# Kernel optimization log

Measured on AMD Instinct MI355X. Metric: run time of the kernel, lower is better.

Reference implementation:

```python
import jax, jax.numpy as jnp
import numpy as np


def setup_inputs() -> dict:
    key = jax.random.key(0)
    ks = jax.random.split(key, 12)
    C, H, L, P = 256, 8, 4, 4
    Lq, Lx = 2048, 300
    iss = jnp.array([[64, 64], [32, 32], [16, 16], [8, 8]], dtype=jnp.int32)
    Len_in = int(np.sum(np.array(iss)[:, 0] * np.array(iss)[:, 1]))  # 5440
    lsi = jnp.array([0, 4096, 5120, 5376], dtype=jnp.int32)
    return {
        "query": jax.random.normal(ks[0], (1, Lq, C), jnp.float32),
        "reference_points": jax.random.uniform(ks[1], (1, Lq, L, 2), jnp.float32),
        "input_flatten": jax.random.normal(ks[2], (1, Len_in, C), jnp.float32),
        "input_spatial_shapes": iss,
        "add_keys": jax.random.normal(ks[3], (1, Lx, C), jnp.float32),
        "input_level_start_index": lsi,
        "W_off": jax.random.normal(ks[4], (H * L * P * 2, C), jnp.float32) * 0.01,
        "b_off": jax.random.normal(ks[5], (H * L * P * 2,), jnp.float32),
        "W_attn": jax.random.normal(ks[6], (H * (L + 1), C, C), jnp.float32) * 0.05,
        "W_v": jax.random.normal(ks[7], (H * 2, C, C), jnp.float32) * 0.05,
        "b_v": jax.random.normal(ks[8], (H * 2, C), jnp.float32) * 0.01,
        "W_mix": jax.random.normal(ks[9], (C, H + 1), jnp.float32) * 0.5,
    }


def reference(query, reference_points, input_flatten, input_spatial_shapes,
              add_keys, input_level_start_index, W_off, b_off, W_attn, W_v, b_v, W_mix):
    N, Lq, C = query.shape
    L = input_spatial_shapes.shape[0]
    H = W_v.shape[0] // 2
    P = W_off.shape[0] // (H * L * 2)

    # sampling locations: ref (x,y in [0,1]) + offsets / (W,H)
    off = (query @ W_off.T + b_off).reshape(N, Lq, H, L, P, 2)
    wh = input_spatial_shapes[:, ::-1].astype(query.dtype)  # (L,2) = (W,H)
    loc = reference_points[:, :, None, :, None, :] + off / wh[None, None, None, :, None, :]

    # get_keys: truncating index computation + gather (faithful to original)
    loc = jnp.clip(loc, 0.0, 0.999)
    iss_f = input_spatial_shapes.astype(loc.dtype)[None, None, None, :, None, :]
    idx = (loc * iss_f).astype(jnp.int32)  # (N,Lq,H,L,P,2): (int(x*H_l), int(y*W_l))
    lin = (idx[..., 0]
           + idx[..., 1] * input_spatial_shapes[:, 0].astype(jnp.int32)[None, None, None, :, None]
           + input_level_start_index.astype(jnp.int32)[None, None, None, :, None])
    keys = input_flatten[0][lin[0]]                # (Lq,H,L,P,C)
    keys = jnp.transpose(keys, (1, 2, 3, 0, 4))    # (H,L,P,Lq,C)

    head_w = jax.nn.softmax(W_mix.T, axis=0)       # (H+1,C)
    qf = query[0]                                  # (Lq,C)
    ak = add_keys[0]                               # (Lx,C)

    # per-head, per-level similarity (replicates original overlapping index h*L+lvl)
    Ws = W_attn[jnp.arange(H)[:, None] * L + jnp.arange(L)[None, :]]  # (H,L,C,C)
    T = jnp.einsum('hlce,hlpqe->hlcpq', Ws, keys)  # (H,L,C,P,Lq)
    # faithful reshape quirk: (C, P*Lq) viewed as (P, Lq, C)
    T = T.reshape(H, L, P, Lq, C)
    attn_s = jnp.einsum('hlpqc,qc->hlpq', T, qf).reshape(H, L * P, Lq)

    Wadd = W_attn[jnp.arange(H) * L + L]           # (H,C,C)
    attn_a = jnp.einsum('xe,hce,qc->hxq', ak, Wadd, qf)  # (H,Lx,Lq)

    attn = jax.nn.softmax(jnp.concatenate([attn_s, attn_a], axis=1), axis=1)
    attn_s_sm, attn_a_sm = attn[:, :L * P], attn[:, L * P:]

    Wv0, bv0 = W_v[0::2], b_v[0::2]
    Wv1, bv1 = W_v[1::2], b_v[1::2]
    vals = (jnp.einsum('hlpqe,hce->hlpqc', keys, Wv0)
            + bv0[:, None, None, None, :]).reshape(H, L * P, Lq, C)
    v2 = jnp.einsum('xe,hce->hxc', ak, Wv1) + bv1[:, None, :]  # (H,Lx,C)

    out_h = (jnp.einsum('hkq,hkqc->hqc', attn_s_sm, vals)
             + jnp.einsum('hxq,hxc->hqc', attn_a_sm, v2))      # (H,Lq,C)
    result = qf * head_w[-1][None, :] + jnp.einsum('hqc,hc->qc', out_h, head_w[:-1])
    return result[None]
```

## Files before the change

### kernel.cpp

```cpp
#include <hip/hip_runtime.h>
#include <stdint.h>

#define NJ 316

typedef __attribute__((ext_vector_type(8))) short short8;
typedef __attribute__((ext_vector_type(4))) float f32x4;
union U4S8 { uint4 u; short8 s; };

__device__ __forceinline__ unsigned short f2bf(float x) {
    unsigned int u = __float_as_uint(x);
    u += 0x7fff + ((u >> 16) & 1);
    return (unsigned short)(u >> 16);
}
__device__ __forceinline__ float bf2f(unsigned short h) {
    return __uint_as_float(((unsigned int)h) << 16);
}

__global__ __launch_bounds__(256) void cvt_all_kernel(
    const float* __restrict__ q,  unsigned short* __restrict__ qh,  unsigned short* __restrict__ ql,
    const float* __restrict__ ak, unsigned short* __restrict__ akh, unsigned short* __restrict__ akl,
    const float* __restrict__ wv, unsigned short* __restrict__ wvh, unsigned short* __restrict__ wvl,
    const float* __restrict__ inflat, unsigned int* __restrict__ inflatP,
    const float* __restrict__ Wattn, unsigned short* __restrict__ wah, unsigned short* __restrict__ wal,
    unsigned short* __restrict__ v2th, unsigned short* __restrict__ v2tl)
{
    int i = blockIdx.x * 256 + threadIdx.x;
    if (i < 760576) {
        const float* s; unsigned short *dh, *dl; int off; bool pack = false;
        unsigned int* dp = nullptr;
        if (i < 131072)      { s = q;  dh = qh;  dl = ql;  off = i; }
        else if (i < 150272) { s = ak; dh = akh; dl = akl; off = i - 131072; }
        else if (i < 412416) { s = wv; dh = wvh; dl = wvl; off = i - 150272; }
        else { s = inflat; dp = inflatP; off = i - 412416; pack = true; dh = dl = nullptr; }
        float4 v = ((const float4*)s)[off];
        float x[4] = {v.x, v.y, v.z, v.w};
        unsigned short h[4], l[4];
        #pragma unroll
        for (int j = 0; j < 4; ++j) {
            h[j] = f2bf(x[j]);
            l[j] = f2bf(x[j] - bf2f(h[j]));
        }
        if (pack) {
            ((uint4*)dp)[off] = make_uint4(
                (unsigned)h[0] | ((unsigned)l[0] << 16),
                (unsigned)h[1] | ((unsigned)l[1] << 16),
                (unsigned)h[2] | ((unsigned)l[2] << 16),
                (unsigned)h[3] | ((unsigned)l[3] << 16));
        } else {
            ((uint2*)dh)[off] = make_uint2((unsigned)h[0] | ((unsigned)h[1] << 16),
                                           (unsigned)h[2] | ((unsigned)h[3] << 16));
            ((uint2*)dl)[off] = make_uint2((unsigned)l[0] | ((unsigned)l[1] << 16),
                                           (unsigned)l[2] | ((unsigned)l[3] << 16));
        }
    } else if (i < 891648) {
        int off = i - 760576;
        int base = off * 4;
        int z = base >> 16, r = base & 65535;
        float4 v = *(const float4*)&Wattn[(size_t)(4 * z + 4) * 65536 + r];
        float x[4] = {v.x, v.y, v.z, v.w};
        unsigned short h[4], l[4];
        #pragma unroll
        for (int j = 0; j < 4; ++j) {
            h[j] = f2bf(x[j]);
            l[j] = f2bf(x[j] - bf2f(h[j]));
        }
        ((uint2*)wah)[off] = make_uint2((unsigned)h[0] | ((unsigned)h[1] << 16),
                                        (unsigned)h[2] | ((unsigned)h[3] << 16));
        ((uint2*)wal)[off] = make_uint2((unsigned)l[0] | ((unsigned)l[1] << 16),
                                        (unsigned)l[2] | ((unsigned)l[3] << 16));
    } else {
        int j = i - 891648;
        size_t base = (size_t)j * 320;
        uint2 zz = make_uint2(0u, 0u);
        #pragma unroll
        for (int d = 0; d < 4; ++d) {
            ((uint2*)(v2th + base))[d] = zz;
            ((uint2*)(v2tl + base))[d] = zz;
        }
        ((uint2*)(v2th + base + 316))[0] = zz;
        ((uint2*)(v2tl + base + 316))[0] = zz;
    }
}

__global__ __launch_bounds__(256) void lin_kernel(
    const float* __restrict__ query, const float* __restrict__ refp,
    const int* __restrict__ iss, const int* __restrict__ lsi,
    const float* __restrict__ Woff, const float* __restrict__ boff,
    int* __restrict__ lin)
{
    __shared__ float qf8[8][256];
    __shared__ float wtile[256][33];
    __shared__ double offl[8][256];
    const int t = threadIdx.x;
    const int qbase = blockIdx.x * 8;
    #pragma unroll
    for (int i = 0; i < 8; ++i) qf8[i][t] = query[(qbase + i) * 256 + t];
    double acc[8];
    #pragma unroll
    for (int r = 0; r < 8; ++r) acc[r] = 0.0;
    for (int cb = 0; cb < 256; cb += 32) {
        __syncthreads();
        #pragma unroll
        for (int i = 0; i < 32; ++i) {
            int f = i * 256 + t;
            int o = f >> 5, jj = f & 31;
            wtile[o][jj] = Woff[o * 256 + cb + jj];
        }
        __syncthreads();
        #pragma unroll
        for (int jj = 0; jj < 32; ++jj) {
            double wv = (double)wtile[t][jj];
            #pragma unroll
            for (int r = 0; r < 8; ++r)
                acc[r] += (double)qf8[r][cb + jj] * wv;
        }
    }
    double bo = (double)boff[t];
    __syncthreads();
    #pragma unroll
    for (int r = 0; r < 8; ++r) offl[r][t] = acc[r] + bo;
    __syncthreads();
    #pragma unroll
    for (int rep = 0; rep < 4; ++rep) {
        int idx = rep * 256 + t;
        int r = idx >> 7;
        int s = idx & 127;
        int l = (s >> 2) & 3;
        int q = qbase + r;
        double offx = offl[r][2 * s];
        double offy = offl[r][2 * s + 1];
        int w0 = iss[l * 2 + 0];
        int w1 = iss[l * 2 + 1];
        double locx = (double)refp[q * 8 + l * 2 + 0] + offx / (double)w1;
        double locy = (double)refp[q * 8 + l * 2 + 1] + offy / (double)w0;
        locx = fmin(fmax(locx, 0.0), 0.999);
        locy = fmin(fmax(locy, 0.0), 0.999);
        int ix = (int)(locx * (double)w0);
        int iy = (int)(locy * (double)w1);
        lin[q * 128 + s] = ix + iy * w0 + lsi[l];
    }
}

__global__ __launch_bounds__(256, 2) void gattn_mfma(
    const unsigned short* __restrict__ qh, const unsigned short* __restrict__ ql,
    const unsigned int* __restrict__ inflatP, const float* __restrict__ Wattn,
    const int* __restrict__ lin, float* __restrict__ attn)
{
    __shared__ int linrow[256];
    __shared__ float Glds[64][268];
    const int t = threadIdx.x;
    const int lane = t & 63, w = t >> 6;
    const int b = blockIdx.x;
    const int qb = b & 7, p = (b >> 3) & 3, l = (b >> 5) & 3, h = b >> 7;
    linrow[t] = lin[(256 * qb + t) * 128 + h * 16 + l * 4 + p];
    __syncthreads();

    const int l15 = lane & 15, g = lane >> 4;
    const int q2l = qb + 8 * p + 32 * l15;
    const int ebase = 64 * w + l15;

    f32x4 acc[4][4];
    #pragma unroll
    for (int i = 0; i < 4; ++i)
        #pragma unroll
        for (int eg = 0; eg < 4; ++eg) acc[i][eg] = (f32x4){0.f, 0.f, 0.f, 0.f};

    for (int kb = 0; kb < 256; kb += 32) {
        U4S8 ah[4], al[4];
        #pragma unroll
        for (int i = 0; i < 4; ++i) {
            size_t off = (size_t)(q2l + 512 * i) * 256 + kb + 8 * g;
            ah[i].u = *(const uint4*)(qh + off);
            al[i].u = *(const uint4*)(ql + off);
        }
        int rowoff[8];
        #pragma unroll
        for (int m = 0; m < 8; ++m) rowoff[m] = linrow[kb + 8 * g + m] * 256;
        unsigned int uv[4][8];
        #pragma unroll
        for (int eg = 0; eg < 4; ++eg)
            #pragma unroll
            for (int m = 0; m < 8; ++m)
                uv[eg][m] = inflatP[rowoff[m] + ebase + 16 * eg];

        #pragma unroll
        for (int eg = 0; eg < 4; ++eg) {
            U4S8 bh, bl;
            unsigned int hh[4], ll[4];
            #pragma unroll
            for (int d = 0; d < 4; ++d) {
                hh[d] = __builtin_amdgcn_perm(uv[eg][2 * d + 1], uv[eg][2 * d],
                                              0x05040100u);
                ll[d] = __builtin_amdgcn_perm(uv[eg][2 * d + 1], uv[eg][2 * d],
                                              0x07060302u);
            }
            bh.u = make_uint4(hh[0], hh[1], hh[2], hh[3]);
            bl.u = make_uint4(ll[0], ll[1], ll[2], ll[3]);
            #pragma unroll
            for (int i = 0; i < 4; ++i) {
                acc[i][eg] = __builtin_amdgcn_mfma_f32_16x16x32_bf16(
                    ah[i].s, bh.s, acc[i][eg], 0, 0, 0);
                acc[i][eg] = __builtin_amdgcn_mfma_f32_16x16x32_bf16(
                    ah[i].s, bl.s, acc[i][eg], 0, 0, 0);
                acc[i][eg] = __builtin_amdgcn_mfma_f32_16x16x32_bf16(
                    al[i].s, bh.s, acc[i][eg], 0, 0, 0);
            }
        }
    }

    #pragma unroll
    for (int i = 0; i < 4; ++i)
        #pragma unroll
        for (int eg = 0; eg < 4; ++eg)
            #pragma unroll
            for (int r = 0; r < 4; ++r)
                Glds[16 * i + 4 * g + r][64 * w + 16 * eg + l15] = acc[i][eg][r];
    __syncthreads();

    const int tx = t & 15, ty = t >> 4;
    const float* Wsbase = Wattn + (size_t)(h * 4 + l) * 65536;
    float gv[4][16];
    #pragma unroll
    for (int r = 0; r < 4; ++r)
        #pragma unroll
        for (int i2 = 0; i2 < 4; ++i2) {
            float4 gd = *(const float4*)&Glds[ty * 4 + r][tx * 4 + 64 * i2];
            gv[r][i2 * 4 + 0] = gd.x;
            gv[r][i2 * 4 + 1] = gd.y;
            gv[r][i2 * 4 + 2] = gd.z;
            gv[r][i2 * 4 + 3] = gd.w;
        }
    #pragma unroll
    for (int r = 0; r < 4; ++r) {
        int hi = ty * 4 + r;
        int q2 = qb + 8 * p + 32 * hi;
        #pragma unroll
        for (int p2 = 0; p2 < 4; ++p2) {
            const float* wr = Wsbase + (size_t)(hi + 64 * p2) * 256;
            float partial = 0.f;
            #pragma unroll
            for (int i2 = 0; i2 < 4; ++i2) {
                float4 wv = *(const float4*)&wr[tx * 4 + 64 * i2];
                partial += wv.x * gv[r][i2 * 4 + 0] + wv.y * gv[r][i2 * 4 + 1]
                         + wv.z * gv[r][i2 * 4 + 2] + wv.w * gv[r][i2 * 4 + 3];
            }
            partial += __shfl_xor(partial, 1);
            partial += __shfl_xor(partial, 2);
            partial += __shfl_xor(partial, 4);
            partial += __shfl_xor(partial, 8);
            if (tx == 0)
                attn[((size_t)h * 2048 + q2) * NJ + (l * 4 + p2)] = partial;
        }
    }
}

struct Seg {
    const unsigned short *Ah, *Al, *Bh, *Bl;
    int K, lda, ldb;
    long sA, sB;
    int nprod;
};

template<bool ACCUM, bool OUTF32, int NSEG>
__device__ __forceinline__ void gemm_core(
    const Seg& s0, const Seg& s1,
    float* __restrict__ Cf, unsigned short* __restrict__ Ch,
    unsigned short* __restrict__ Cl,
    int M, int N, int ldc, long sC, int nb, int mb, int z)
{
    __shared__ unsigned short As[2][64 * 40];
    __shared__ unsigned short Bs[2][128 * 40];
    const int t = threadIdx.x;
    const int lane = t & 63;
    const int wave = t >> 6;
    const int wm = (wave & 1) * 32, wn = (wave >> 1) * 64;

    f32x4 acc[2][4];
    #pragma unroll
    for (int i = 0; i < 2; ++i)
        #pragma unroll
        for (int j = 0; j < 4; ++j) acc[i][j] = (f32x4){0.f, 0.f, 0.f, 0.f};

    const int arow = t >> 2, akoff = (t & 3) * 8;
    const int frow = lane & 15, fk = (lane >> 4) * 8;

    #pragma unroll
    for (int seg = 0; seg < NSEG; ++seg) {
        const Seg S = seg ? s1 : s0;
        const int np = S.nprod;
        const unsigned short* Azh = S.Ah + (size_t)z * S.sA;
        const unsigned short* Azl = (np >= 2) ? S.Al + (size_t)z * S.sA : nullptr;
        const unsigned short* Bzh = S.Bh + (size_t)z * S.sB;
        const unsigned short* Bzl = (np >= 3) ? S.Bl + (size_t)z * S.sB : nullptr;
        for (int kb = 0; kb < S.K; kb += 32) {
            __syncthreads();
            {
                int gm = mb + arow;
                uint4 vh = {0, 0, 0, 0}, vl = {0, 0, 0, 0};
                if (gm < M) {
                    size_t o = (size_t)gm * S.lda + kb + akoff;
                    vh = *(const uint4*)(Azh + o);
                    if (np >= 2) vl = *(const uint4*)(Azl + o);
                }
                *(uint4*)&As[0][arow * 40 + akoff] = vh;
                if (np >= 2) *(uint4*)&As[1][arow * 40 + akoff] = vl;
                #pragma unroll
                for (int i = 0; i < 2; ++i) {
                    int f = i * 256 + t;
                    int brow = f >> 2, bkoff = (f & 3) * 8;
                    int gn = nb + brow;
                    uint4 wh = {0, 0, 0, 0}, wl = {0, 0, 0, 0};
                    if (gn < N) {
                        size_t o = (size_t)gn * S.ldb + kb + bkoff;
                        wh = *(const uint4*)(Bzh + o);
                        if (np >= 3) wl = *(const uint4*)(Bzl + o);
                    }
                    *(uint4*)&Bs[0][brow * 40 + bkoff] = wh;
                    if (np >= 3) *(uint4*)&Bs[1][brow * 40 + bkoff] = wl;
                }
            }
            __syncthreads();
            short8 a[2][2], b[4][2];
            #pragma unroll
            for (int i = 0; i < 2; ++i) {
                int r = wm + i * 16 + frow;
                a[i][0] = *(const short8*)&As[0][r * 40 + fk];
                if (np >= 2) a[i][1] = *(const short8*)&As[1][r * 40 + fk];
            }
            #pragma unroll
            for (int j = 0; j < 4; ++j) {
                int r = wn + j * 16 + frow;
                b[j][0] = *(const short8*)&Bs[0][r * 40 + fk];
                if (np >= 3) b[j][1] = *(const short8*)&Bs[1][r * 40 + fk];
            }
            #pragma unroll
            for (int i = 0; i < 2; ++i)
                #pragma unroll
                for (int j = 0; j < 4; ++j) {
                    acc[i][j] = __builtin_amdgcn_mfma_f32_16x16x32_bf16(
                        a[i][0], b[j][0], acc[i][j], 0, 0, 0);
                    if (np >= 2)
                        acc[i][j] = __builtin_amdgcn_mfma_f32_16x16x32_bf16(
                            a[i][1], b[j][0], acc[i][j], 0, 0, 0);
                    if (np >= 3)
                        acc[i][j] = __builtin_amdgcn_mfma_f32_16x16x32_bf16(
                            a[i][0], b[j][1], acc[i][j], 0, 0, 0);
                }
        }
    }
    #pragma unroll
    for (int i = 0; i < 2; ++i)
        #pragma unroll
        for (int r = 0; r < 4; ++r) {
            int gm = mb + wm + i * 16 + (lane >> 4) * 4 + r;
            if (gm >= M) continue;
            #pragma unroll
            for (int j = 0; j < 4; ++j) {
                int gn = nb + wn + j * 16 + (lane & 15);
                if (gn >= N) continue;
                size_t idx = (size_t)z * sC + (size_t)gm * ldc + gn;
                float v = acc[i][j][r];
                if (OUTF32) {
                    float prev = ACCUM ? Cf[idx] : 0.f;
                    Cf[idx] = prev + v;
                } else {
                    unsigned short h = f2bf(v);
                    Ch[idx] = h;
                    Cl[idx] = f2bf(v - bf2f(h));
                }
            }
        }
}

template<bool ACCUM, bool OUTF32, int NSEG>
__global__ __launch_bounds__(256) void mfma_gemm(
    Seg s0, Seg s1,
    float* __restrict__ Cf, unsigned short* __restrict__ Ch,
    unsigned short* __restrict__ Cl,
    int M, int N, int ldc, long sC)
{
    gemm_core<ACCUM, OUTF32, NSEG>(s0, s1, Cf, Ch, Cl, M, N, ldc, sC,
                                   blockIdx.x * 128, blockIdx.y * 64,
                                   blockIdx.z);
}

__global__ __launch_bounds__(256) void mfma_gemm_dual(
    Seg a, int Ma, int Na, int ldca, long sCa,
    unsigned short* __restrict__ Cha, unsigned short* __restrict__ Cla,
    Seg b, int Mb, int Nb, int ldcb, long sCb,
    unsigned short* __restrict__ Chb, unsigned short* __restrict__ Clb,
    int ax)
{
    Seg dummy = a;
    if ((int)blockIdx.x < ax) {
        if ((int)blockIdx.y * 64 >= Ma) return;
        gemm_core<false, false, 1>(a, dummy, nullptr, Cha, Cla,
                                   Ma, Na, ldca, sCa,
                                   blockIdx.x * 128, blockIdx.y * 64,
                                   blockIdx.z);
    } else {
        if ((int)blockIdx.y * 64 >= Mb) return;
        gemm_core<false, false, 1>(b, dummy, nullptr, Chb, Clb,
                                   Mb, Nb, ldcb, sCb,
                                   (blockIdx.x - ax) * 128, blockIdx.y * 64,
                                   blockIdx.z);
    }
}

__global__ __launch_bounds__(256) void softmax_ka_kernel(
    const float* __restrict__ attn, const unsigned int* __restrict__ inflatP,
    const int* __restrict__ lin, float* __restrict__ s0,
    unsigned short* __restrict__ awh,
    unsigned short* __restrict__ KAh, unsigned short* __restrict__ KAl)
{
    __shared__ float red[8];
    __shared__ float w16[16];
    __shared__ int lls[16];
    const int t = threadIdx.x;
    const int lane = t & 63, w = t >> 6;
    const int rid = blockIdx.x;
    const int h = rid >> 11, q = rid & 2047;
    const float* row = attn + (size_t)rid * NJ;

    float v0 = row[t];
    float v1 = (t < 60) ? row[256 + t] : -1e30f;
    float m = fmaxf(v0, v1);
    #pragma unroll
    for (int d = 1; d < 64; d <<= 1) m = fmaxf(m, __shfl_xor(m, d));
    if (lane == 0) red[w] = m;
    __syncthreads();
    m = fmaxf(fmaxf(red[0], red[1]), fmaxf(red[2], red[3]));

    float e0 = expf(v0 - m);
    float e1 = (t < 60) ? expf(v1 - m) : 0.f;
    float s = e0 + e1;
    #pragma unroll
    for (int d = 1; d < 64; d <<= 1) s += __shfl_xor(s, d);
    if (lane == 0) red[4 + w] = s;
    __syncthreads();
    s = (red[4] + red[5]) + (red[6] + red[7]);
    const float inv = 1.f / s;

    float sf = (t < 16) ? e0 : 0.f;
    #pragma unroll
    for (int d = 1; d < 64; d <<= 1) sf += __shfl_xor(sf, d);
    if (lane == 0) red[w] = sf;

    float a0 = e0 * inv;
    float a1 = (t < 60) ? e1 * inv : 0.f;
    awh[(size_t)rid * 320 + t] = f2bf(a0);
    if (t < 64)
        awh[(size_t)rid * 320 + 256 + t] = f2bf(a1);
    if (t < 16) {
        w16[t] = a0;
        lls[t] = lin[q * 128 + h * 16 + t];
    }
    __syncthreads();
    if (t == 0)
        s0[rid] = ((red[0] + red[1]) + (red[2] + red[3])) * inv;

    float acc = 0.f;
    #pragma unroll
    for (int k = 0; k < 16; ++k) {
        unsigned int u = inflatP[lls[k] * 256 + t];
        acc += w16[k] * (bf2f((unsigned short)(u & 0xffff)) +
                         bf2f((unsigned short)(u >> 16)));
    }
    unsigned short hh = f2bf(acc);
    KAh[(size_t)rid * 256 + t] = hh;
    KAl[(size_t)rid * 256 + t] = f2bf(acc - bf2f(hh));
}

__global__ __launch_bounds__(256) void final_kernel(
    const float* __restrict__ qf, const float* __restrict__ OH,
    const float* __restrict__ s0, const float* __restrict__ bv,
    const float* __restrict__ Wmix, float* __restrict__ out)
{
    const int q = blockIdx.x, c = threadIdx.x;
    float wj[9], m = -1e30f;
    #pragma unroll
    for (int j = 0; j < 9; ++j) { wj[j] = Wmix[c * 9 + j]; m = fmaxf(m, wj[j]); }
    float s = 0.f;
    #pragma unroll
    for (int j = 0; j < 9; ++j) { wj[j] = expf(wj[j] - m); s += wj[j]; }
    float inv = 1.f / s;
    float acc = qf[q * 256 + c] * wj[8] * inv;
    #pragma unroll
    for (int h = 0; h < 8; ++h) {
        float s0v = s0[h * 2048 + q];
        float oh = OH[((size_t)h * 2048 + q) * 256 + c]
                 + s0v * bv[(2 * h) * 256 + c]
                 + (1.f - s0v) * bv[(2 * h + 1) * 256 + c];
        acc += oh * wj[h] * inv;
    }
    out[q * 256 + c] = acc;
}

extern "C" void kernel_launch(void* const* d_in, const int* in_sizes, int n_in,
                              void* d_out, int out_size, void* d_ws, size_t ws_size,
                              hipStream_t stream) {
    const float* query = (const float*)d_in[0];
    const float* refp  = (const float*)d_in[1];
    const float* inflat= (const float*)d_in[2];
    const int*   iss   = (const int*)d_in[3];
    const float* ak    = (const float*)d_in[4];
    const int*   lsi   = (const int*)d_in[5];
    const float* Woff  = (const float*)d_in[6];
    const float* boff  = (const float*)d_in[7];
    const float* Wattn = (const float*)d_in[8];
    const float* Wv    = (const float*)d_in[9];
    const float* bv    = (const float*)d_in[10];
    const float* Wmix  = (const float*)d_in[11];
    float* out = (float*)d_out;

    typedef unsigned short us;
    char* ws = (char*)d_ws;
    int* lin    = (int*)ws;   ws += (size_t)262144 * 4;
    float* attn = (float*)ws; ws += (size_t)8 * 2048 * NJ * 4;
    float* s0   = (float*)ws; ws += (size_t)8 * 2048 * 4;
    unsigned int* inflatP = (unsigned int*)ws; ws += (size_t)1392640 * 4;
    us* qh  = (us*)ws; ws += (size_t)524288 * 2;
    us* ql  = (us*)ws; ws += (size_t)524288 * 2;
    us* akh = (us*)ws; ws += (size_t)320 * 256 * 2;
    us* akl = (us*)ws; ws += (size_t)320 * 256 * 2;
    us* Waddh = (us*)ws; ws += (size_t)524288 * 2;
    us* Waddl = (us*)ws; ws += (size_t)524288 * 2;
    us* Wvh = (us*)ws; ws += (size_t)1048576 * 2;
    us* Wvl = (us*)ws; ws += (size_t)1048576 * 2;
    us* Bhh = (us*)ws; ws += (size_t)8 * 320 * 256 * 2;
    us* Bhl = (us*)ws; ws += (size_t)8 * 320 * 256 * 2;
    us* V2Th= (us*)ws; ws += (size_t)8 * 256 * 320 * 2;
    us* V2Tl= (us*)ws; ws += (size_t)8 * 256 * 320 * 2;
    us* awh = (us*)ws; ws += (size_t)8 * 2048 * 320 * 2;
    us* KAh = (us*)ws; ws += (size_t)8 * 2048 * 256 * 2;
    us* KAl = (us*)ws; ws += (size_t)8 * 2048 * 256 * 2;
    float* OH = (float*)ws;   ws += (size_t)8 * 2048 * 256 * 4;

    cvt_all_kernel<<<3491, 256, 0, stream>>>(
        query, qh, ql, ak, akh, akl, Wv, Wvh, Wvl,
        inflat, inflatP, Wattn, Waddh, Waddl, V2Th, V2Tl);
    lin_kernel<<<256, 256, 0, stream>>>(query, refp, iss, lsi, Woff, boff, lin);

    Seg sz = {nullptr, nullptr, nullptr, nullptr, 0, 0, 0, 0L, 0L, 0};

    {
        Seg a = {akh, akl, Waddh, Waddl, 256, 256, 256, 0L, 65536L, 3};
        Seg b = {Wvh + 65536, Wvl + 65536, akh, nullptr, 256, 256, 256,
                 131072L, 0L, 2};
        mfma_gemm_dual<<<dim3(5, 5, 8), 256, 0, stream>>>(
            a, 300, 256, 256, 320L * 256, Bhh, Bhl,
            b, 256, 300, 320, 256L * 320, V2Th + 16, V2Tl + 16, 2);
    }
    {
        Seg a = {qh, ql, Bhh, Bhl, 256, 256, 256, 0L, 320L * 256, 3};
        mfma_gemm<false, true, 1><<<dim3(3, 32, 8), 256, 0, stream>>>(
            a, sz, attn + 16, nullptr, nullptr, 2048, 300, NJ, 2048L * NJ);
    }

    gattn_mfma<<<1024, 256, 0, stream>>>(qh, ql, inflatP, Wattn, lin, attn);

    softmax_ka_kernel<<<16384, 256, 0, stream>>>(attn, inflatP, lin, s0,
                                                 awh, KAh, KAl);

    {
        Seg a = {KAh, KAl, Wvh, nullptr, 256, 256, 256, 2048L * 256,
                 2L * 65536, 2};
        Seg b = {awh, nullptr, V2Th, nullptr, 320, 320, 320, 2048L * 320,
                 256L * 320, 1};
        mfma_gemm<false, true, 2><<<dim3(2, 32, 8), 256, 0, stream>>>(
            a, b, OH, nullptr, nullptr, 2048, 256, 256, 2048L * 256);
    }

    final_kernel<<<2048, 256, 0, stream>>>(query, OH, s0, bv, Wmix, out);
}
```

Before: 268.7 us.

## Merge conversion with offset kernel and gather-attn with attn-add GEMM launches

The conversion kernel and the sampling-offset kernel become one launch, with extra blocks running the offset/lin computation. The gather-attention kernel and the attn-add GEMM are also combined into a single launch of 1792 blocks, using shared memory passed into gemm_core. This removes two launches and lets independent work overlap within one grid. The cost is that the shared-memory allocation (69.6KB) applies to every block, including GEMM blocks, which may cut occupancy. The offset kernel's weight tile was also halved to 16 columns.

```diff
diff --git a/kernel.cpp b/kernel.cpp
--- a/kernel.cpp
+++ b/kernel.cpp
@@ -14,244 +14,6 @@
 }
 __device__ __forceinline__ float bf2f(unsigned short h) {
     return __uint_as_float(((unsigned int)h) << 16);
-}
-
-__global__ __launch_bounds__(256) void cvt_all_kernel(
-    const float* __restrict__ q,  unsigned short* __restrict__ qh,  unsigned short* __restrict__ ql,
-    const float* __restrict__ ak, unsigned short* __restrict__ akh, unsigned short* __restrict__ akl,
-    const float* __restrict__ wv, unsigned short* __restrict__ wvh, unsigned short* __restrict__ wvl,
-    const float* __restrict__ inflat, unsigned int* __restrict__ inflatP,
-    const float* __restrict__ Wattn, unsigned short* __restrict__ wah, unsigned short* __restrict__ wal,
-    unsigned short* __restrict__ v2th, unsigned short* __restrict__ v2tl)
-{
-    int i = blockIdx.x * 256 + threadIdx.x;
-    if (i < 760576) {
-        const float* s; unsigned short *dh, *dl; int off; bool pack = false;
-        unsigned int* dp = nullptr;
-        if (i < 131072)      { s = q;  dh = qh;  dl = ql;  off = i; }
-        else if (i < 150272) { s = ak; dh = akh; dl = akl; off = i - 131072; }
-        else if (i < 412416) { s = wv; dh = wvh; dl = wvl; off = i - 150272; }
-        else { s = inflat; dp = inflatP; off = i - 412416; pack = true; dh = dl = nullptr; }
-        float4 v = ((const float4*)s)[off];
-        float x[4] = {v.x, v.y, v.z, v.w};
-        unsigned short h[4], l[4];
-        #pragma unroll
-        for (int j = 0; j < 4; ++j) {
-            h[j] = f2bf(x[j]);
-            l[j] = f2bf(x[j] - bf2f(h[j]));
-        }
-        if (pack) {
-            ((uint4*)dp)[off] = make_uint4(
-                (unsigned)h[0] | ((unsigned)l[0] << 16),
-                (unsigned)h[1] | ((unsigned)l[1] << 16),
-                (unsigned)h[2] | ((unsigned)l[2] << 16),
-                (unsigned)h[3] | ((unsigned)l[3] << 16));
-        } else {
-            ((uint2*)dh)[off] = make_uint2((unsigned)h[0] | ((unsigned)h[1] << 16),
-                                           (unsigned)h[2] | ((unsigned)h[3] << 16));
-            ((uint2*)dl)[off] = make_uint2((unsigned)l[0] | ((unsigned)l[1] << 16),
-                                           (unsigned)l[2] | ((unsigned)l[3] << 16));
-        }
-    } else if (i < 891648) {
-        int off = i - 760576;
-        int base = off * 4;
-        int z = base >> 16, r = base & 65535;
-        float4 v = *(const float4*)&Wattn[(size_t)(4 * z + 4) * 65536 + r];
-        float x[4] = {v.x, v.y, v.z, v.w};
-        unsigned short h[4], l[4];
-        #pragma unroll
-        for (int j = 0; j < 4; ++j) {
-            h[j] = f2bf(x[j]);
-            l[j] = f2bf(x[j] - bf2f(h[j]));
-        }
-        ((uint2*)wah)[off] = make_uint2((unsigned)h[0] | ((unsigned)h[1] << 16),
-                                        (unsigned)h[2] | ((unsigned)h[3] << 16));
-        ((uint2*)wal)[off] = make_uint2((unsigned)l[0] | ((unsigned)l[1] << 16),
-                                        (unsigned)l[2] | ((unsigned)l[3] << 16));
-    } else {
-        int j = i - 891648;
-        size_t base = (size_t)j * 320;
-        uint2 zz = make_uint2(0u, 0u);
-        #pragma unroll
-        for (int d = 0; d < 4; ++d) {
-            ((uint2*)(v2th + base))[d] = zz;
-            ((uint2*)(v2tl + base))[d] = zz;
-        }
-        ((uint2*)(v2th + base + 316))[0] = zz;
-        ((uint2*)(v2tl + base + 316))[0] = zz;
-    }
-}
-
-__global__ __launch_bounds__(256) void lin_kernel(
-    const float* __restrict__ query, const float* __restrict__ refp,
-    const int* __restrict__ iss, const int* __restrict__ lsi,
-    const float* __restrict__ Woff, const float* __restrict__ boff,
-    int* __restrict__ lin)
-{
-    __shared__ float qf8[8][256];
-    __shared__ float wtile[256][33];
-    __shared__ double offl[8][256];
-    const int t = threadIdx.x;
-    const int qbase = blockIdx.x * 8;
-    #pragma unroll
-    for (int i = 0; i < 8; ++i) qf8[i][t] = query[(qbase + i) * 256 + t];
-    double acc[8];
-    #pragma unroll
-    for (int r = 0; r < 8; ++r) acc[r] = 0.0;
-    for (int cb = 0; cb < 256; cb += 32) {
-        __syncthreads();
-        #pragma unroll
-        for (int i = 0; i < 32; ++i) {
-            int f = i * 256 + t;
-            int o = f >> 5, jj = f & 31;
-            wtile[o][jj] = Woff[o * 256 + cb + jj];
-        }
-        __syncthreads();
-        #pragma unroll
-        for (int jj = 0; jj < 32; ++jj) {
-            double wv = (double)wtile[t][jj];
-            #pragma unroll
-            for (int r = 0; r < 8; ++r)
-                acc[r] += (double)qf8[r][cb + jj] * wv;
-        }
-    }
-    double bo = (double)boff[t];
-    __syncthreads();
-    #pragma unroll
-    for (int r = 0; r < 8; ++r) offl[r][t] = acc[r] + bo;
-    __syncthreads();
-    #pragma unroll
-    for (int rep = 0; rep < 4; ++rep) {
-        int idx = rep * 256 + t;
-        int r = idx >> 7;
-        int s = idx & 127;
-        int l = (s >> 2) & 3;
-        int q = qbase + r;
-        double offx = offl[r][2 * s];
-        double offy = offl[r][2 * s + 1];
-        int w0 = iss[l * 2 + 0];
-        int w1 = iss[l * 2 + 1];
-        double locx = (double)refp[q * 8 + l * 2 + 0] + offx / (double)w1;
-        double locy = (double)refp[q * 8 + l * 2 + 1] + offy / (double)w0;
-        locx = fmin(fmax(locx, 0.0), 0.999);
-        locy = fmin(fmax(locy, 0.0), 0.999);
-        int ix = (int)(locx * (double)w0);
-        int iy = (int)(locy * (double)w1);
-        lin[q * 128 + s] = ix + iy * w0 + lsi[l];
-    }
-}
-
-__global__ __launch_bounds__(256, 2) void gattn_mfma(
-    const unsigned short* __restrict__ qh, const unsigned short* __restrict__ ql,
-    const unsigned int* __restrict__ inflatP, const float* __restrict__ Wattn,
-    const int* __restrict__ lin, float* __restrict__ attn)
-{
-    __shared__ int linrow[256];
-    __shared__ float Glds[64][268];
-    const int t = threadIdx.x;
-    const int lane = t & 63, w = t >> 6;
-    const int b = blockIdx.x;
-    const int qb = b & 7, p = (b >> 3) & 3, l = (b >> 5) & 3, h = b >> 7;
-    linrow[t] = lin[(256 * qb + t) * 128 + h * 16 + l * 4 + p];
-    __syncthreads();
-
-    const int l15 = lane & 15, g = lane >> 4;
-    const int q2l = qb + 8 * p + 32 * l15;
-    const int ebase = 64 * w + l15;
-
-    f32x4 acc[4][4];
-    #pragma unroll
-    for (int i = 0; i < 4; ++i)
-        #pragma unroll
-        for (int eg = 0; eg < 4; ++eg) acc[i][eg] = (f32x4){0.f, 0.f, 0.f, 0.f};
-
-    for (int kb = 0; kb < 256; kb += 32) {
-        U4S8 ah[4], al[4];
-        #pragma unroll
-        for (int i = 0; i < 4; ++i) {
-            size_t off = (size_t)(q2l + 512 * i) * 256 + kb + 8 * g;
-            ah[i].u = *(const uint4*)(qh + off);
-            al[i].u = *(const uint4*)(ql + off);
-        }
-        int rowoff[8];
-        #pragma unroll
-        for (int m = 0; m < 8; ++m) rowoff[m] = linrow[kb + 8 * g + m] * 256;
-        unsigned int uv[4][8];
-        #pragma unroll
-        for (int eg = 0; eg < 4; ++eg)
-            #pragma unroll
-            for (int m = 0; m < 8; ++m)
-                uv[eg][m] = inflatP[rowoff[m] + ebase + 16 * eg];
-
-        #pragma unroll
-        for (int eg = 0; eg < 4; ++eg) {
-            U4S8 bh, bl;
-            unsigned int hh[4], ll[4];
-            #pragma unroll
-            for (int d = 0; d < 4; ++d) {
-                hh[d] = __builtin_amdgcn_perm(uv[eg][2 * d + 1], uv[eg][2 * d],
-                                              0x05040100u);
-                ll[d] = __builtin_amdgcn_perm(uv[eg][2 * d + 1], uv[eg][2 * d],
-                                              0x07060302u);
-            }
-            bh.u = make_uint4(hh[0], hh[1], hh[2], hh[3]);
-            bl.u = make_uint4(ll[0], ll[1], ll[2], ll[3]);
-            #pragma unroll
-            for (int i = 0; i < 4; ++i) {
-                acc[i][eg] = __builtin_amdgcn_mfma_f32_16x16x32_bf16(
-                    ah[i].s, bh.s, acc[i][eg], 0, 0, 0);
-                acc[i][eg] = __builtin_amdgcn_mfma_f32_16x16x32_bf16(
-                    ah[i].s, bl.s, acc[i][eg], 0, 0, 0);
-                acc[i][eg] = __builtin_amdgcn_mfma_f32_16x16x32_bf16(
-                    al[i].s, bh.s, acc[i][eg], 0, 0, 0);
-            }
-        }
-    }
-
-    #pragma unroll
-    for (int i = 0; i < 4; ++i)
-        #pragma unroll
-        for (int eg = 0; eg < 4; ++eg)
-            #pragma unroll
-            for (int r = 0; r < 4; ++r)
-                Glds[16 * i + 4 * g + r][64 * w + 16 * eg + l15] = acc[i][eg][r];
-    __syncthreads();
-
-    const int tx = t & 15, ty = t >> 4;
-    const float* Wsbase = Wattn + (size_t)(h * 4 + l) * 65536;
-    float gv[4][16];
-    #pragma unroll
-    for (int r = 0; r < 4; ++r)
-        #pragma unroll
-        for (int i2 = 0; i2 < 4; ++i2) {
-            float4 gd = *(const float4*)&Glds[ty * 4 + r][tx * 4 + 64 * i2];
-            gv[r][i2 * 4 + 0] = gd.x;
-            gv[r][i2 * 4 + 1] = gd.y;
-            gv[r][i2 * 4 + 2] = gd.z;
-            gv[r][i2 * 4 + 3] = gd.w;
-        }
-    #pragma unroll
-    for (int r = 0; r < 4; ++r) {
-        int hi = ty * 4 + r;
-        int q2 = qb + 8 * p + 32 * hi;
-        #pragma unroll
-        for (int p2 = 0; p2 < 4; ++p2) {
-            const float* wr = Wsbase + (size_t)(hi + 64 * p2) * 256;
-            float partial = 0.f;
-            #pragma unroll
-            for (int i2 = 0; i2 < 4; ++i2) {
-                float4 wv = *(const float4*)&wr[tx * 4 + 64 * i2];
-                partial += wv.x * gv[r][i2 * 4 + 0] + wv.y * gv[r][i2 * 4 + 1]
-                         + wv.z * gv[r][i2 * 4 + 2] + wv.w * gv[r][i2 * 4 + 3];
-            }
-            partial += __shfl_xor(partial, 1);
-            partial += __shfl_xor(partial, 2);
-            partial += __shfl_xor(partial, 4);
-            partial += __shfl_xor(partial, 8);
-            if (tx == 0)
-                attn[((size_t)h * 2048 + q2) * NJ + (l * 4 + p2)] = partial;
-        }
-    }
 }
 
 struct Seg {
@@ -266,10 +28,10 @@
     const Seg& s0, const Seg& s1,
     float* __restrict__ Cf, unsigned short* __restrict__ Ch,
     unsigned short* __restrict__ Cl,
-    int M, int N, int ldc, long sC, int nb, int mb, int z)
-{
-    __shared__ unsigned short As[2][64 * 40];
-    __shared__ unsigned short Bs[2][128 * 40];
+    int M, int N, int ldc, long sC, int nb, int mb, int z, char* smem)
+{
+    unsigned short* As0 = (unsigned short*)smem;
+    unsigned short* Bs0 = (unsigned short*)(smem + 10240);
     const int t = threadIdx.x;
     const int lane = t & 63;
     const int wave = t >> 6;
@@ -302,8 +64,8 @@
                     vh = *(const uint4*)(Azh + o);
                     if (np >= 2) vl = *(const uint4*)(Azl + o);
                 }
-                *(uint4*)&As[0][arow * 40 + akoff] = vh;
-                if (np >= 2) *(uint4*)&As[1][arow * 40 + akoff] = vl;
+                *(uint4*)&As0[arow * 40 + akoff] = vh;
+                if (np >= 2) *(uint4*)&As0[2560 + arow * 40 + akoff] = vl;
                 #pragma unroll
                 for (int i = 0; i < 2; ++i) {
                     int f = i * 256 + t;
@@ -315,8 +77,8 @@
                         wh = *(const uint4*)(Bzh + o);
                         if (np >= 3) wl = *(const uint4*)(Bzl + o);
                     }
-                    *(uint4*)&Bs[0][brow * 40 + bkoff] = wh;
-                    if (np >= 3) *(uint4*)&Bs[1][brow * 40 + bkoff] = wl;
+                    *(uint4*)&Bs0[brow * 40 + bkoff] = wh;
+                    if (np >= 3) *(uint4*)&Bs0[5120 + brow * 40 + bkoff] = wl;
                 }
             }
             __syncthreads();
@@ -324,14 +86,14 @@
             #pragma unroll
             for (int i = 0; i < 2; ++i) {
                 int r = wm + i * 16 + frow;
-                a[i][0] = *(const short8*)&As[0][r * 40 + fk];
-                if (np >= 2) a[i][1] = *(const short8*)&As[1][r * 40 + fk];
+                a[i][0] = *(const short8*)&As0[r * 40 + fk];
+                if (np >= 2) a[i][1] = *(const short8*)&As0[2560 + r * 40 + fk];
             }
             #pragma unroll
             for (int j = 0; j < 4; ++j) {
                 int r = wn + j * 16 + frow;
-                b[j][0] = *(const short8*)&Bs[0][r * 40 + fk];
-                if (np >= 3) b[j][1] = *(const short8*)&Bs[1][r * 40 + fk];
+                b[j][0] = *(const short8*)&Bs0[r * 40 + fk];
+                if (np >= 3) b[j][1] = *(const short8*)&Bs0[5120 + r * 40 + fk];
             }
             #pragma unroll
             for (int i = 0; i < 2; ++i)
@@ -379,9 +141,10 @@
     unsigned short* __restrict__ Cl,
     int M, int N, int ldc, long sC)
 {
+    __shared__ __align__(16) char smem[30720];
     gemm_core<ACCUM, OUTF32, NSEG>(s0, s1, Cf, Ch, Cl, M, N, ldc, sC,
                                    blockIdx.x * 128, blockIdx.y * 64,
-                                   blockIdx.z);
+                                   blockIdx.z, smem);
 }
 
 __global__ __launch_bounds__(256) void mfma_gemm_dual(
@@ -391,19 +154,269 @@
     unsigned short* __restrict__ Chb, unsigned short* __restrict__ Clb,
     int ax)
 {
+    __shared__ __align__(16) char smem[30720];
     Seg dummy = a;
     if ((int)blockIdx.x < ax) {
         if ((int)blockIdx.y * 64 >= Ma) return;
         gemm_core<false, false, 1>(a, dummy, nullptr, Cha, Cla,
                                    Ma, Na, ldca, sCa,
                                    blockIdx.x * 128, blockIdx.y * 64,
-                                   blockIdx.z);
+                                   blockIdx.z, smem);
     } else {
         if ((int)blockIdx.y * 64 >= Mb) return;
         gemm_core<false, false, 1>(b, dummy, nullptr, Chb, Clb,
                                    Mb, Nb, ldcb, sCb,
                                    (blockIdx.x - ax) * 128, blockIdx.y * 64,
-                                   blockIdx.z);
+                                   blockIdx.z, smem);
+    }
+}
+
+__global__ __launch_bounds__(256) void cvt_lin_kernel(
+    const float* __restrict__ q,  unsigned short* __restrict__ qh,  unsigned short* __restrict__ ql,
+    const float* __restrict__ ak, unsigned short* __restrict__ akh, unsigned short* __restrict__ akl,
+    const float* __restrict__ wv, unsigned short* __restrict__ wvh, unsigned short* __restrict__ wvl,
+    const float* __restrict__ inflat, unsigned int* __restrict__ inflatP,
+    const float* __restrict__ Wattn, unsigned short* __restrict__ wah, unsigned short* __restrict__ wal,
+    unsigned short* __restrict__ v2th, unsigned short* __restrict__ v2tl,
+    const float* __restrict__ refp, const int* __restrict__ iss,
+    const int* __restrict__ lsi, const float* __restrict__ Woff,
+    const float* __restrict__ boff, int* __restrict__ lin)
+{
+    __shared__ float qf8[8][256];
+    __shared__ float wtile[256][17];
+    __shared__ double offl[8][256];
+    const int t = threadIdx.x;
+
+    if (blockIdx.x < 3491) {
+        int i = blockIdx.x * 256 + t;
+        if (i < 760576) {
+            const float* s; unsigned short *dh, *dl; int off; bool pack = false;
+            unsigned int* dp = nullptr;
+            if (i < 131072)      { s = q;  dh = qh;  dl = ql;  off = i; }
+            else if (i < 150272) { s = ak; dh = akh; dl = akl; off = i - 131072; }
+            else if (i < 412416) { s = wv; dh = wvh; dl = wvl; off = i - 150272; }
+            else { s = inflat; dp = inflatP; off = i - 412416; pack = true; dh = dl = nullptr; }
+            float4 v = ((const float4*)s)[off];
+            float x[4] = {v.x, v.y, v.z, v.w};
+            unsigned short h[4], l[4];
+            #pragma unroll
+            for (int j = 0; j < 4; ++j) {
+                h[j] = f2bf(x[j]);
+                l[j] = f2bf(x[j] - bf2f(h[j]));
+            }
+            if (pack) {
+                ((uint4*)dp)[off] = make_uint4(
+                    (unsigned)h[0] | ((unsigned)l[0] << 16),
+                    (unsigned)h[1] | ((unsigned)l[1] << 16),
+                    (unsigned)h[2] | ((unsigned)l[2] << 16),
+                    (unsigned)h[3] | ((unsigned)l[3] << 16));
+            } else {
+                ((uint2*)dh)[off] = make_uint2((unsigned)h[0] | ((unsigned)h[1] << 16),
+                                               (unsigned)h[2] | ((unsigned)h[3] << 16));
+                ((uint2*)dl)[off] = make_uint2((unsigned)l[0] | ((unsigned)l[1] << 16),
+                                               (unsigned)l[2] | ((unsigned)l[3] << 16));
+            }
+        } else if (i < 891648) {
+            int off = i - 760576;
+            int base = off * 4;
+            int z = base >> 16, r = base & 65535;
+            float4 v = *(const float4*)&Wattn[(size_t)(4 * z + 4) * 65536 + r];
+            float x[4] = {v.x, v.y, v.z, v.w};
+            unsigned short h[4], l[4];
+            #pragma unroll
+            for (int j = 0; j < 4; ++j) {
+                h[j] = f2bf(x[j]);
+                l[j] = f2bf(x[j] - bf2f(h[j]));
+            }
+            ((uint2*)wah)[off] = make_uint2((unsigned)h[0] | ((unsigned)h[1] << 16),
+                                            (unsigned)h[2] | ((unsigned)h[3] << 16));
+            ((uint2*)wal)[off] = make_uint2((unsigned)l[0] | ((unsigned)l[1] << 16),
+                                            (unsigned)l[2] | ((unsigned)l[3] << 16));
+        } else {
+            int j = i - 891648;
+            size_t base = (size_t)j * 320;
+            uint2 zz = make_uint2(0u, 0u);
+            #pragma unroll
+            for (int d = 0; d < 4; ++d) {
+                ((uint2*)(v2th + base))[d] = zz;
+                ((uint2*)(v2tl + base))[d] = zz;
+            }
+            ((uint2*)(v2th + base + 316))[0] = zz;
+            ((uint2*)(v2tl + base + 316))[0] = zz;
+        }
+        return;
+    }
+
+    const int qbase = (blockIdx.x - 3491) * 8;
+    #pragma unroll
+    for (int i = 0; i < 8; ++i) qf8[i][t] = q[(qbase + i) * 256 + t];
+    double acc[8];
+    #pragma unroll
+    for (int r = 0; r < 8; ++r) acc[r] = 0.0;
+    for (int cb = 0; cb < 256; cb += 16) {
+        __syncthreads();
+        #pragma unroll
+        for (int i = 0; i < 16; ++i) {
+            int f = i * 256 + t;
+            int o = f >> 4, jj = f & 15;
+            wtile[o][jj] = Woff[o * 256 + cb + jj];
+        }
+        __syncthreads();
+        #pragma unroll
+        for (int jj = 0; jj < 16; ++jj) {
+            double wvv = (double)wtile[t][jj];
+            #pragma unroll
+            for (int r = 0; r < 8; ++r)
+                acc[r] += (double)qf8[r][cb + jj] * wvv;
+        }
+    }
+    double bo = (double)boff[t];
+    __syncthreads();
+    #pragma unroll
+    for (int r = 0; r < 8; ++r) offl[r][t] = acc[r] + bo;
+    __syncthreads();
+    #pragma unroll
+    for (int rep = 0; rep < 4; ++rep) {
+        int idx = rep * 256 + t;
+        int r = idx >> 7;
+        int s = idx & 127;
+        int l = (s >> 2) & 3;
+        int qq = qbase + r;
+        double offx = offl[r][2 * s];
+        double offy = offl[r][2 * s + 1];
+        int w0 = iss[l * 2 + 0];
+        int w1 = iss[l * 2 + 1];
+        double locx = (double)refp[qq * 8 + l * 2 + 0] + offx / (double)w1;
+        double locy = (double)refp[qq * 8 + l * 2 + 1] + offy / (double)w0;
+        locx = fmin(fmax(locx, 0.0), 0.999);
+        locy = fmin(fmax(locy, 0.0), 0.999);
+        int ix = (int)(locx * (double)w0);
+        int iy = (int)(locy * (double)w1);
+        lin[qq * 128 + s] = ix + iy * w0 + lsi[l];
+    }
+}
+
+__global__ __launch_bounds__(256, 2) void gattn_attnA(
+    const unsigned short* __restrict__ qh, const unsigned short* __restrict__ ql,
+    const unsigned int* __restrict__ inflatP, const float* __restrict__ Wattn,
+    const int* __restrict__ lin, float* __restrict__ attn, Seg aA)
+{
+    __shared__ __align__(16) char smem[69632];
+    const int t = threadIdx.x;
+
+    if ((int)blockIdx.x >= 1024) {
+        int idx = blockIdx.x - 1024;
+        int z = idx & 7, my = (idx >> 3) & 31, nx = idx >> 8;
+        gemm_core<false, true, 1>(aA, aA, attn + 16, nullptr, nullptr,
+                                  2048, 300, NJ, 2048L * NJ,
+                                  nx * 128, my * 64, z, smem);
+        return;
+    }
+
+    int* linrow = (int*)smem;
+    float (*Glds)[268] = (float(*)[268])(smem + 1024);
+    const int lane = t & 63, w = t >> 6;
+    const int b = blockIdx.x;
+    const int qb = b & 7, p = (b >> 3) & 3, l = (b >> 5) & 3, h = b >> 7;
+    linrow[t] = lin[(256 * qb + t) * 128 + h * 16 + l * 4 + p];
+    __syncthreads();
+
+    const int l15 = lane & 15, g = lane >> 4;
+    const int q2l = qb + 8 * p + 32 * l15;
+    const int ebase = 64 * w + l15;
+
+    f32x4 acc[4][4];
+    #pragma unroll
+    for (int i = 0; i < 4; ++i)
+        #pragma unroll
+        for (int eg = 0; eg < 4; ++eg) acc[i][eg] = (f32x4){0.f, 0.f, 0.f, 0.f};
+
+    for (int kb = 0; kb < 256; kb += 32) {
+        U4S8 ah[4], al[4];
+        #pragma unroll
+        for (int i = 0; i < 4; ++i) {
+            size_t off = (size_t)(q2l + 512 * i) * 256 + kb + 8 * g;
+            ah[i].u = *(const uint4*)(qh + off);
+            al[i].u = *(const uint4*)(ql + off);
+        }
+        int rowoff[8];
+        #pragma unroll
+        for (int m = 0; m < 8; ++m) rowoff[m] = linrow[kb + 8 * g + m] * 256;
+        unsigned int uv[4][8];
+        #pragma unroll
+        for (int eg = 0; eg < 4; ++eg)
+            #pragma unroll
+            for (int m = 0; m < 8; ++m)
+                uv[eg][m] = inflatP[rowoff[m] + ebase + 16 * eg];
+
+        #pragma unroll
+        for (int eg = 0; eg < 4; ++eg) {
+            U4S8 bh, bl;
+            unsigned int hh[4], ll[4];
+            #pragma unroll
+            for (int d = 0; d < 4; ++d) {
+                hh[d] = __builtin_amdgcn_perm(uv[eg][2 * d + 1], uv[eg][2 * d],
+                                              0x05040100u);
+                ll[d] = __builtin_amdgcn_perm(uv[eg][2 * d + 1], uv[eg][2 * d],
+                                              0x07060302u);
+            }
+            bh.u = make_uint4(hh[0], hh[1], hh[2], hh[3]);
+            bl.u = make_uint4(ll[0], ll[1], ll[2], ll[3]);
+            #pragma unroll
+            for (int i = 0; i < 4; ++i) {
+                acc[i][eg] = __builtin_amdgcn_mfma_f32_16x16x32_bf16(
+                    ah[i].s, bh.s, acc[i][eg], 0, 0, 0);
+                acc[i][eg] = __builtin_amdgcn_mfma_f32_16x16x32_bf16(
+                    ah[i].s, bl.s, acc[i][eg], 0, 0, 0);
+                acc[i][eg] = __builtin_amdgcn_mfma_f32_16x16x32_bf16(
+                    al[i].s, bh.s, acc[i][eg], 0, 0, 0);
+            }
+        }
+    }
+
+    #pragma unroll
+    for (int i = 0; i < 4; ++i)
+        #pragma unroll
+        for (int eg = 0; eg < 4; ++eg)
+            #pragma unroll
+            for (int r = 0; r < 4; ++r)
+                Glds[16 * i + 4 * g + r][64 * w + 16 * eg + l15] = acc[i][eg][r];
+    __syncthreads();
+
+    const int tx = t & 15, ty = t >> 4;
+    const float* Wsbase = Wattn + (size_t)(h * 4 + l) * 65536;
+    float gv[4][16];
+    #pragma unroll
+    for (int r = 0; r < 4; ++r)
+        #pragma unroll
+        for (int i2 = 0; i2 < 4; ++i2) {
+            float4 gd = *(const float4*)&Glds[ty * 4 + r][tx * 4 + 64 * i2];
+            gv[r][i2 * 4 + 0] = gd.x;
+            gv[r][i2 * 4 + 1] = gd.y;
+            gv[r][i2 * 4 + 2] = gd.z;
+            gv[r][i2 * 4 + 3] = gd.w;
+        }
+    #pragma unroll
+    for (int r = 0; r < 4; ++r) {
+        int hi = ty * 4 + r;
+        int q2 = qb + 8 * p + 32 * hi;
+        #pragma unroll
+        for (int p2 = 0; p2 < 4; ++p2) {
+            const float* wr = Wsbase + (size_t)(hi + 64 * p2) * 256;
+            float partial = 0.f;
+            #pragma unroll
+            for (int i2 = 0; i2 < 4; ++i2) {
+                float4 wv = *(const float4*)&wr[tx * 4 + 64 * i2];
+                partial += wv.x * gv[r][i2 * 4 + 0] + wv.y * gv[r][i2 * 4 + 1]
+                         + wv.z * gv[r][i2 * 4 + 2] + wv.w * gv[r][i2 * 4 + 3];
+            }
+            partial += __shfl_xor(partial, 1);
+            partial += __shfl_xor(partial, 2);
+            partial += __shfl_xor(partial, 4);
+            partial += __shfl_xor(partial, 8);
+            if (tx == 0)
+                attn[((size_t)h * 2048 + q2) * NJ + (l * 4 + p2)] = partial;
+        }
     }
 }
 
@@ -536,10 +549,10 @@
     us* KAl = (us*)ws; ws += (size_t)8 * 2048 * 256 * 2;
     float* OH = (float*)ws;   ws += (size_t)8 * 2048 * 256 * 4;
 
-    cvt_all_kernel<<<3491, 256, 0, stream>>>(
+    cvt_lin_kernel<<<3747, 256, 0, stream>>>(
         query, qh, ql, ak, akh, akl, Wv, Wvh, Wvl,
-        inflat, inflatP, Wattn, Waddh, Waddl, V2Th, V2Tl);
-    lin_kernel<<<256, 256, 0, stream>>>(query, refp, iss, lsi, Woff, boff, lin);
+        inflat, inflatP, Wattn, Waddh, Waddl, V2Th, V2Tl,
+        refp, iss, lsi, Woff, boff, lin);
 
     Seg sz = {nullptr, nullptr, nullptr, nullptr, 0, 0, 0, 0L, 0L, 0};
 
@@ -551,13 +564,12 @@
             a, 300, 256, 256, 320L * 256, Bhh, Bhl,
             b, 256, 300, 320, 256L * 320, V2Th + 16, V2Tl + 16, 2);
     }
+
     {
-        Seg a = {qh, ql, Bhh, Bhl, 256, 256, 256, 0L, 320L * 256, 3};
-        mfma_gemm<false, true, 1><<<dim3(3, 32, 8), 256, 0, stream>>>(
-            a, sz, attn + 16, nullptr, nullptr, 2048, 300, NJ, 2048L * NJ);
-    }
-
-    gattn_mfma<<<1024, 256, 0, stream>>>(qh, ql, inflatP, Wattn, lin, attn);
+        Seg aA = {qh, ql, Bhh, Bhl, 256, 256, 256, 0L, 320L * 256, 3};
+        gattn_attnA<<<1792, 256, 0, stream>>>(qh, ql, inflatP, Wattn, lin,
+                                              attn, aA);
+    }
 
     softmax_ka_kernel<<<16384, 256, 0, stream>>>(attn, inflatP, lin, s0,
                                                  awh, KAh, KAl);
```

After: 310.1 us. 1.15x slower.
